# Kernel optimization log

Hardware: AMD Instinct MI355X
Metric: run time of the kernel (lower is better)

Reference implementation:

```python
import jax, jax.numpy as jnp
import numpy as np

N_NODES = 10000
N_EDGES = 320000
F = 256


def setup_inputs() -> dict:
    key = jax.random.key(0)
    ks = jax.random.split(key, 8)
    node_feats = jax.random.normal(ks[0], (N_NODES, F), dtype=jnp.float32)
    edge_feats = jax.random.normal(ks[1], (N_EDGES, F), dtype=jnp.float32)
    src = jax.random.randint(ks[2], (N_EDGES,), 0, N_NODES, dtype=jnp.int64)
    dst = jax.random.randint(ks[3], (N_EDGES,), 0, N_NODES, dtype=jnp.int64)
    scale = 1.0 / np.sqrt(F)
    W_src = jax.random.uniform(ks[4], (1, F), jnp.float32, -scale, scale)
    W_dst = jax.random.uniform(ks[5], (1, F), jnp.float32, -scale, scale)
    W_edge = jax.random.uniform(ks[6], (1, F), jnp.float32, -scale, scale)
    b_src = jnp.zeros((1,), jnp.float32)
    b_dst = jnp.zeros((1,), jnp.float32)
    b_edge = jnp.zeros((1,), jnp.float32)
    return {
        "node_feats": node_feats, "edge_feats": edge_feats,
        "src": src, "dst": dst,
        "W_src": W_src, "b_src": b_src,
        "W_dst": W_dst, "b_dst": b_dst,
        "W_edge": W_edge, "b_edge": b_edge,
    }


def reference(node_feats, edge_feats, src, dst,
              W_src, b_src, W_dst, b_dst, W_edge, b_edge):
    # per-node gate projections: [N, out]
    e_src = node_feats @ W_src.T + b_src
    e_dst = node_feats @ W_dst.T + b_dst
    # u_add_v edge gather + edge gate linear, fused elementwise: [E, out]
    m = e_src[src] + e_dst[dst] + (edge_feats @ W_edge.T + b_edge)
    return jax.nn.sigmoid(m)
```

## Files before the change

kernel.cpp:

```cpp
#include <hip/hip_runtime.h>
#include <math.h>


#define FDIM 256
#define F4   64

typedef float f32x4 __attribute__((ext_vector_type(4)));

__device__ __forceinline__ float dot4v(f32x4 a, f32x4 b) {
    return a[0] * b[0] + a[1] * b[1] + a[2] * b[2] + a[3] * b[3];
}

__global__ void node_gates_kernel(const float* __restrict__ nf,
                                  const float* __restrict__ W_src,
                                  const float* __restrict__ W_dst,
                                  const float* __restrict__ b_src,
                                  const float* __restrict__ b_dst,
                                  float* __restrict__ e_src,
                                  float* __restrict__ e_dst,
                                  int n_nodes) {
    const int lane   = threadIdx.x & 63;
    const int sub    = lane >> 4;
    const int i      = lane & 15;
    const int wave   = (blockIdx.x * blockDim.x + threadIdx.x) >> 6;
    const int nwaves = (gridDim.x * blockDim.x) >> 6;

    const f32x4* Ws4 = reinterpret_cast<const f32x4*>(W_src);
    const f32x4* Wd4 = reinterpret_cast<const f32x4*>(W_dst);
    const f32x4 ws0 = Ws4[i], ws1 = Ws4[i + 16], ws2 = Ws4[i + 32], ws3 = Ws4[i + 48];
    const f32x4 wd0 = Wd4[i], wd1 = Wd4[i + 16], wd2 = Wd4[i + 32], wd3 = Wd4[i + 48];
    const float bs = b_src[0];
    const float bd = b_dst[0];

    const int ngroups = (n_nodes + 3) >> 2;
    for (int g = wave; g < ngroups; g += nwaves) {
        const int n = g * 4 + sub;
        if (n >= n_nodes) continue;
        const f32x4* row = reinterpret_cast<const f32x4*>(nf) + (size_t)n * F4;
        const f32x4 x0 = row[i], x1 = row[i + 16], x2 = row[i + 32], x3 = row[i + 48];
        float ss = dot4v(x0, ws0) + dot4v(x1, ws1) + dot4v(x2, ws2) + dot4v(x3, ws3);
        float sd = dot4v(x0, wd0) + dot4v(x1, wd1) + dot4v(x2, wd2) + dot4v(x3, wd3);
        #pragma unroll
        for (int off = 1; off < 16; off <<= 1) {
            ss += __shfl_xor(ss, off, 64);
            sd += __shfl_xor(sd, off, 64);
        }
        if (i == 0) {
            e_src[n] = ss + bs;
            e_dst[n] = sd + bd;
        }
    }
}

__global__ void __launch_bounds__(256, 8)
edge_gate_kernel(const float* __restrict__ ef,
                 const int* __restrict__ src,
                 const int* __restrict__ dst,
                 const float* __restrict__ W_edge,
                 const float* __restrict__ b_edge,
                 const float* __restrict__ e_src,
                 const float* __restrict__ e_dst,
                 float* __restrict__ out,
                 int n_edges) {
    const int lane   = threadIdx.x & 63;
    const int sub    = lane >> 4;
    const int i      = lane & 15;
    const int wave   = (blockIdx.x * blockDim.x + threadIdx.x) >> 6;
    const int nwaves = (gridDim.x * blockDim.x) >> 6;

    const f32x4* We4 = reinterpret_cast<const f32x4*>(W_edge);
    const f32x4 w0 = We4[i], w1 = We4[i + 16], w2 = We4[i + 32], w3 = We4[i + 48];
    const float be = b_edge[0];

    const f32x4* ef4 = reinterpret_cast<const f32x4*>(ef);
    const int ngroups = (n_edges + 3) >> 2;

    int g = wave;
    if (g >= ngroups) return;

    f32x4 x0, x1, x2, x3;
    {
        const int e = g * 4 + sub;
        if (e < n_edges) {
            const f32x4* row = ef4 + (size_t)e * F4;
            x0 = __builtin_nontemporal_load(row + i);
            x1 = __builtin_nontemporal_load(row + i + 16);
            x2 = __builtin_nontemporal_load(row + i + 32);
            x3 = __builtin_nontemporal_load(row + i + 48);
        } else {
            x0 = x1 = x2 = x3 = (f32x4)0.f;
        }
    }

    while (g < ngroups) {
        const int gn = g + nwaves;
        f32x4 y0, y1, y2, y3;
        if (gn < ngroups) {
            const int en = gn * 4 + sub;
            if (en < n_edges) {
                const f32x4* row = ef4 + (size_t)en * F4;
                y0 = __builtin_nontemporal_load(row + i);
                y1 = __builtin_nontemporal_load(row + i + 16);
                y2 = __builtin_nontemporal_load(row + i + 32);
                y3 = __builtin_nontemporal_load(row + i + 48);
            } else {
                y0 = y1 = y2 = y3 = (f32x4)0.f;
            }
        }

        float s = dot4v(x0, w0) + dot4v(x1, w1) + dot4v(x2, w2) + dot4v(x3, w3);
        #pragma unroll
        for (int off = 1; off < 16; off <<= 1) {
            s += __shfl_xor(s, off, 64);
        }
        const int e = g * 4 + sub;
        if (i == 0 && e < n_edges) {
            const float m = s + be + e_src[src[e]] + e_dst[dst[e]];
            out[e] = 1.0f / (1.0f + __expf(-m));
        }

        g = gn;
        x0 = y0; x1 = y1; x2 = y2; x3 = y3;
    }
}

extern "C" void kernel_launch(void* const* d_in, const int* in_sizes, int n_in,
                              void* d_out, int out_size, void* d_ws, size_t ws_size,
                              hipStream_t stream) {
    const float* node_feats = (const float*)d_in[0];
    const float* edge_feats = (const float*)d_in[1];
    const int*   src        = (const int*)d_in[2];
    const int*   dst        = (const int*)d_in[3];
    const float* W_src      = (const float*)d_in[4];
    const float* b_src      = (const float*)d_in[5];
    const float* W_dst      = (const float*)d_in[6];
    const float* b_dst      = (const float*)d_in[7];
    const float* W_edge     = (const float*)d_in[8];
    const float* b_edge     = (const float*)d_in[9];

    const int n_nodes = in_sizes[0] / FDIM;
    const int n_edges = in_sizes[2];

    float* e_src = (float*)d_ws;
    float* e_dst = e_src + n_nodes;

    {
        int ngroups = (n_nodes + 3) / 4;
        int blocks = (ngroups + 3) / 4;
        if (blocks > 2048) blocks = 2048;
        node_gates_kernel<<<blocks, 256, 0, stream>>>(
            node_feats, W_src, W_dst, b_src, b_dst, e_src, e_dst, n_nodes);
    }

    {
        edge_gate_kernel<<<2048, 256, 0, stream>>>(
            edge_feats, src, dst, W_edge, b_edge, e_src, e_dst,
            (float*)d_out, n_edges);
    }
}
```

Baseline: 59.48 us.

## Fuse node and edge dot products into one kernel, move gather to epilogue

Node-gate and edge-gate dot products now run in a single kernel. The first waves compute the node gates while also prefetching their first edge rows, and the edge loop's starting groups are rotated so those waves begin on the tail groups. The edge dot products are written to a workspace buffer. A second lightweight kernel then gathers e_src/e_dst by index and applies the sigmoid. This removes the serial dependency between the node kernel and the large edge-streaming kernel, at the cost of an extra write and read of an E-sized intermediate and one more launch.

```diff
diff --git a/kernel.cpp b/kernel.cpp
--- a/kernel.cpp
+++ b/kernel.cpp
@@ -11,57 +11,14 @@
     return a[0] * b[0] + a[1] * b[1] + a[2] * b[2] + a[3] * b[3];
 }
 
-__global__ void node_gates_kernel(const float* __restrict__ nf,
-                                  const float* __restrict__ W_src,
-                                  const float* __restrict__ W_dst,
-                                  const float* __restrict__ b_src,
-                                  const float* __restrict__ b_dst,
-                                  float* __restrict__ e_src,
-                                  float* __restrict__ e_dst,
-                                  int n_nodes) {
-    const int lane   = threadIdx.x & 63;
-    const int sub    = lane >> 4;
-    const int i      = lane & 15;
-    const int wave   = (blockIdx.x * blockDim.x + threadIdx.x) >> 6;
-    const int nwaves = (gridDim.x * blockDim.x) >> 6;
-
-    const f32x4* Ws4 = reinterpret_cast<const f32x4*>(W_src);
-    const f32x4* Wd4 = reinterpret_cast<const f32x4*>(W_dst);
-    const f32x4 ws0 = Ws4[i], ws1 = Ws4[i + 16], ws2 = Ws4[i + 32], ws3 = Ws4[i + 48];
-    const f32x4 wd0 = Wd4[i], wd1 = Wd4[i + 16], wd2 = Wd4[i + 32], wd3 = Wd4[i + 48];
-    const float bs = b_src[0];
-    const float bd = b_dst[0];
-
-    const int ngroups = (n_nodes + 3) >> 2;
-    for (int g = wave; g < ngroups; g += nwaves) {
-        const int n = g * 4 + sub;
-        if (n >= n_nodes) continue;
-        const f32x4* row = reinterpret_cast<const f32x4*>(nf) + (size_t)n * F4;
-        const f32x4 x0 = row[i], x1 = row[i + 16], x2 = row[i + 32], x3 = row[i + 48];
-        float ss = dot4v(x0, ws0) + dot4v(x1, ws1) + dot4v(x2, ws2) + dot4v(x3, ws3);
-        float sd = dot4v(x0, wd0) + dot4v(x1, wd1) + dot4v(x2, wd2) + dot4v(x3, wd3);
-        #pragma unroll
-        for (int off = 1; off < 16; off <<= 1) {
-            ss += __shfl_xor(ss, off, 64);
-            sd += __shfl_xor(sd, off, 64);
-        }
-        if (i == 0) {
-            e_src[n] = ss + bs;
-            e_dst[n] = sd + bd;
-        }
-    }
-}
-
 __global__ void __launch_bounds__(256, 8)
-edge_gate_kernel(const float* __restrict__ ef,
-                 const int* __restrict__ src,
-                 const int* __restrict__ dst,
-                 const float* __restrict__ W_edge,
-                 const float* __restrict__ b_edge,
-                 const float* __restrict__ e_src,
-                 const float* __restrict__ e_dst,
-                 float* __restrict__ out,
-                 int n_edges) {
+fused_dots_kernel(const float* __restrict__ nf, const float* __restrict__ ef,
+                  const float* __restrict__ W_src, const float* __restrict__ b_src,
+                  const float* __restrict__ W_dst, const float* __restrict__ b_dst,
+                  const float* __restrict__ W_edge, const float* __restrict__ b_edge,
+                  float* __restrict__ e_src, float* __restrict__ e_dst,
+                  float* __restrict__ gdef,
+                  int n_nodes, int n_edges, int ng_node) {
     const int lane   = threadIdx.x & 63;
     const int sub    = lane >> 4;
     const int i      = lane & 15;
@@ -75,37 +32,54 @@
     const f32x4* ef4 = reinterpret_cast<const f32x4*>(ef);
     const int ngroups = (n_edges + 3) >> 2;
 
-    int g = wave;
-    if (g >= ngroups) return;
+    int g = (wave < ng_node) ? (wave + nwaves - ng_node) : (wave - ng_node);
 
     f32x4 x0, x1, x2, x3;
-    {
-        const int e = g * 4 + sub;
-        if (e < n_edges) {
-            const f32x4* row = ef4 + (size_t)e * F4;
-            x0 = __builtin_nontemporal_load(row + i);
-            x1 = __builtin_nontemporal_load(row + i + 16);
-            x2 = __builtin_nontemporal_load(row + i + 32);
-            x3 = __builtin_nontemporal_load(row + i + 48);
-        } else {
-            x0 = x1 = x2 = x3 = (f32x4)0.f;
+    const bool have_first = (g < ngroups);
+    if (have_first) {
+        const f32x4* row = ef4 + (size_t)(g * 4 + sub) * F4;
+        x0 = __builtin_nontemporal_load(row + i);
+        x1 = __builtin_nontemporal_load(row + i + 16);
+        x2 = __builtin_nontemporal_load(row + i + 32);
+        x3 = __builtin_nontemporal_load(row + i + 48);
+    } else {
+        x0 = x1 = x2 = x3 = (f32x4)0.f;
+    }
+
+    if (wave < ng_node) {
+        const int n = wave * 4 + sub;
+        const f32x4* Ws4 = reinterpret_cast<const f32x4*>(W_src);
+        const f32x4* Wd4 = reinterpret_cast<const f32x4*>(W_dst);
+        const f32x4* row = reinterpret_cast<const f32x4*>(nf) + (size_t)n * F4;
+        const f32x4 a0 = row[i], a1 = row[i + 16], a2 = row[i + 32], a3 = row[i + 48];
+        float ss = dot4v(a0, Ws4[i])      + dot4v(a1, Ws4[i + 16])
+                 + dot4v(a2, Ws4[i + 32]) + dot4v(a3, Ws4[i + 48]);
+        float sd = dot4v(a0, Wd4[i])      + dot4v(a1, Wd4[i + 16])
+                 + dot4v(a2, Wd4[i + 32]) + dot4v(a3, Wd4[i + 48]);
+        #pragma unroll
+        for (int off = 1; off < 16; off <<= 1) {
+            ss += __shfl_xor(ss, off, 64);
+            sd += __shfl_xor(sd, off, 64);
+        }
+        if (i == 0 && n < n_nodes) {
+            e_src[n] = ss + b_src[0];
+            e_dst[n] = sd + b_dst[0];
         }
     }
+
+    if (!have_first) return;
 
     while (g < ngroups) {
         const int gn = g + nwaves;
         f32x4 y0, y1, y2, y3;
         if (gn < ngroups) {
-            const int en = gn * 4 + sub;
-            if (en < n_edges) {
-                const f32x4* row = ef4 + (size_t)en * F4;
-                y0 = __builtin_nontemporal_load(row + i);
-                y1 = __builtin_nontemporal_load(row + i + 16);
-                y2 = __builtin_nontemporal_load(row + i + 32);
-                y3 = __builtin_nontemporal_load(row + i + 48);
-            } else {
-                y0 = y1 = y2 = y3 = (f32x4)0.f;
-            }
+            const f32x4* row = ef4 + (size_t)(gn * 4 + sub) * F4;
+            y0 = __builtin_nontemporal_load(row + i);
+            y1 = __builtin_nontemporal_load(row + i + 16);
+            y2 = __builtin_nontemporal_load(row + i + 32);
+            y3 = __builtin_nontemporal_load(row + i + 48);
+        } else {
+            y0 = y1 = y2 = y3 = (f32x4)0.f;
         }
 
         float s = dot4v(x0, w0) + dot4v(x1, w1) + dot4v(x2, w2) + dot4v(x3, w3);
@@ -115,12 +89,25 @@
         }
         const int e = g * 4 + sub;
         if (i == 0 && e < n_edges) {
-            const float m = s + be + e_src[src[e]] + e_dst[dst[e]];
-            out[e] = 1.0f / (1.0f + __expf(-m));
+            gdef[e] = s + be;
         }
 
         g = gn;
         x0 = y0; x1 = y1; x2 = y2; x3 = y3;
+    }
+}
+
+__global__ void edge_epilogue_kernel(const float* __restrict__ gdef,
+                                     const int* __restrict__ src,
+                                     const int* __restrict__ dst,
+                                     const float* __restrict__ e_src,
+                                     const float* __restrict__ e_dst,
+                                     float* __restrict__ out,
+                                     int n_edges) {
+    const int e = blockIdx.x * blockDim.x + threadIdx.x;
+    if (e < n_edges) {
+        const float m = gdef[e] + e_src[src[e]] + e_dst[dst[e]];
+        out[e] = 1.0f / (1.0f + __expf(-m));
     }
 }
 
@@ -140,21 +127,17 @@
 
     const int n_nodes = in_sizes[0] / FDIM;
     const int n_edges = in_sizes[2];
+    const int ng_node = (n_nodes + 3) / 4;
 
     float* e_src = (float*)d_ws;
     float* e_dst = e_src + n_nodes;
+    float* gdef  = e_dst + n_nodes;
 
-    {
-        int ngroups = (n_nodes + 3) / 4;
-        int blocks = (ngroups + 3) / 4;
-        if (blocks > 2048) blocks = 2048;
-        node_gates_kernel<<<blocks, 256, 0, stream>>>(
-            node_feats, W_src, W_dst, b_src, b_dst, e_src, e_dst, n_nodes);
-    }
+    fused_dots_kernel<<<2048, 256, 0, stream>>>(
+        node_feats, edge_feats,
+        W_src, b_src, W_dst, b_dst, W_edge, b_edge,
+        e_src, e_dst, gdef, n_nodes, n_edges, ng_node);
 
-    {
-        edge_gate_kernel<<<2048, 256, 0, stream>>>(
-            edge_feats, src, dst, W_edge, b_edge, e_src, e_dst,
-            (float*)d_out, n_edges);
-    }
+    edge_epilogue_kernel<<<(n_edges + 255) / 256, 256, 0, stream>>>(
+        gdef, src, dst, e_src, e_dst, (float*)d_out, n_edges);
 }
```

Result: no change. 59.69 us (+0.4%).
